# Performance work log

Hardware: AMD Instinct MI355X
Metric: run time of the kernel (lower is better)

Reference implementation:

```python
import jax, jax.numpy as jnp
import numpy as np

SEQ, B, D_IN, H = 512, 64, 256, 1024

def setup_inputs() -> dict:
    key = jax.random.key(0)
    k1, k2, k3, k4 = jax.random.split(key, 4)
    x = jax.random.normal(k1, (SEQ, B, D_IN), dtype=jnp.float32)
    W_in = jax.random.normal(k2, (H, D_IN), dtype=jnp.float32) / np.sqrt(D_IN)
    W_hh = jax.random.normal(k3, (H, H), dtype=jnp.float32) / np.sqrt(H)
    bias = jnp.zeros((H,), dtype=jnp.float32)
    alpha = jax.random.uniform(k4, (H,), dtype=jnp.float32)
    return {"x": x, "W_in": W_in, "W_hh": W_hh, "bias": bias, "alpha": alpha}

def reference(x, W_in, W_hh, bias, alpha):
    # x: [S, B, D_in]; returns (output [S, B, H], h_n [B, H])
    S, B_, _ = x.shape
    H_ = W_hh.shape[0]
    # Precompute input projection for all timesteps in one GEMM: [S, B, H]
    x_proj = jnp.einsum('sbi,hi->sbh', x, W_in) + bias

    def step(h_prev, xp_t):
        h_tilde = jnp.tanh(xp_t + h_prev @ W_hh.T)
        h = (1.0 - alpha) * h_prev + alpha * h_tilde
        return h, h

    h0 = jnp.zeros((B_, H_), dtype=x.dtype)
    h_n, output = jax.lax.scan(step, h0, x_proj)
    return output, h_n
```

## Files before the change

### kernel.cpp

```cpp
#include <hip/hip_runtime.h>
#include <hip/hip_cooperative_groups.h>
#include <cstdint>
#include <cstddef>

#define SEQ   512
#define BATCH 64
#define DIN   256
#define HDIM  1024
#define NGROUP 8
#define GROWS  8
#define NSLAB  32

typedef __attribute__((ext_vector_type(8)))  short  short8;
typedef __attribute__((ext_vector_type(4)))  float  float4v;
typedef __attribute__((ext_vector_type(2)))  float  float2v;

__device__ __forceinline__ short f2bf(float f) {
    union { float f; uint32_t u; } v; v.f = f;
    uint32_t u = v.u;
    uint32_t r = (u + 0x7fffu + ((u >> 16) & 1u)) >> 16;
    return (short)(r & 0xffffu);
}
__device__ __forceinline__ float bf2f(short s) {
    union { uint32_t u; float f; } v; v.u = ((uint32_t)(uint16_t)s) << 16;
    return v.f;
}

__global__ void prep_kernel(const float* __restrict__ W_hh,
                            short* __restrict__ w_hi,
                            short* __restrict__ w_lo,
                            short* __restrict__ hbuf,
                            unsigned int* __restrict__ prog) {
    int tid = blockIdx.x * blockDim.x + threadIdx.x;
    int stride = gridDim.x * blockDim.x;
    for (int i = tid; i < HDIM * HDIM; i += stride) {
        float w = W_hh[i];
        short hi = f2bf(w);
        float lo = w - bf2f(hi);
        w_hi[i] = hi;
        w_lo[i] = f2bf(lo);
    }
    for (int i = tid; i < 2 * BATCH * HDIM; i += stride) hbuf[i] = 0;
    for (int i = tid; i < NGROUP * NSLAB; i += stride) prog[i] = 0u;
}

#define XBM 128
#define XBN 128
#define XBK 32

__global__ __launch_bounds__(256) void xproj_kernel(
    const float* __restrict__ X,
    const float* __restrict__ Win,
    const float* __restrict__ bias,
    float* __restrict__ out)
{
    __shared__ float As[XBK][XBM + 4];
    __shared__ float Bs[XBK][XBN + 4];
    const int bm = blockIdx.x;
    const int bn = blockIdx.y;
    const int r0 = bm * XBM, c0 = bn * XBN;
    const int tid = threadIdx.x;
    const int tx = tid & 15, ty = tid >> 4;

    float acc[8][8];
#pragma unroll
    for (int i = 0; i < 8; i++)
#pragma unroll
        for (int j = 0; j < 8; j++) acc[i][j] = 0.f;

    for (int k0 = 0; k0 < DIN; k0 += XBK) {
#pragma unroll
        for (int r = 0; r < 4; r++) {
            int row = (tid >> 3) + 32 * r;
            int kk  = (tid & 7) * 4;
            float4v v = *(const float4v*)(X + (size_t)(r0 + row) * DIN + k0 + kk);
            As[kk + 0][row] = v[0]; As[kk + 1][row] = v[1];
            As[kk + 2][row] = v[2]; As[kk + 3][row] = v[3];
        }
#pragma unroll
        for (int r = 0; r < 4; r++) {
            int row = (tid >> 3) + 32 * r;
            int kk  = (tid & 7) * 4;
            float4v v = *(const float4v*)(Win + (size_t)(c0 + row) * DIN + k0 + kk);
            Bs[kk + 0][row] = v[0]; Bs[kk + 1][row] = v[1];
            Bs[kk + 2][row] = v[2]; Bs[kk + 3][row] = v[3];
        }
        __syncthreads();
#pragma unroll
        for (int k = 0; k < XBK; k++) {
            float4v a0 = *(const float4v*)&As[k][ty * 8];
            float4v a1 = *(const float4v*)&As[k][ty * 8 + 4];
            float4v b0 = *(const float4v*)&Bs[k][tx * 8];
            float4v b1 = *(const float4v*)&Bs[k][tx * 8 + 4];
            float a[8] = {a0[0],a0[1],a0[2],a0[3],a1[0],a1[1],a1[2],a1[3]};
            float b[8] = {b0[0],b0[1],b0[2],b0[3],b1[0],b1[1],b1[2],b1[3]};
#pragma unroll
            for (int i = 0; i < 8; i++)
#pragma unroll
                for (int j = 0; j < 8; j++) acc[i][j] += a[i] * b[j];
        }
        __syncthreads();
    }

    float4v ba = *(const float4v*)(bias + c0 + tx * 8);
    float4v bb = *(const float4v*)(bias + c0 + tx * 8 + 4);
#pragma unroll
    for (int i = 0; i < 8; i++) {
        size_t row = (size_t)(r0 + ty * 8 + i);
        float4v v0, v1;
#pragma unroll
        for (int j = 0; j < 4; j++) { v0[j] = acc[i][j] + ba[j]; v1[j] = acc[i][4 + j] + bb[j]; }
        *(float4v*)(out + row * HDIM + c0 + tx * 8)     = v0;
        *(float4v*)(out + row * HDIM + c0 + tx * 8 + 4) = v1;
    }
}

__global__ __launch_bounds__(512, 2) void rnn2_kernel(
    const float* __restrict__ alpha,
    const short* __restrict__ w_hi,
    const short* __restrict__ w_lo,
    short* __restrict__ hbuf,
    unsigned int* __restrict__ prog,
    float* __restrict__ out)
{
    __shared__ float zbuf[8][2][16][16];

    const int blk  = blockIdx.x;
    const int g    = blk >> 5;
    const int j    = blk & 31;
    const int tid  = threadIdx.x;
    const int wave = tid >> 6;
    const int lane = tid & 63;
    const int kq   = wave;
    const int ln15 = lane & 15;
    const int kg   = lane >> 4;
    const int k_base = kq * 128 + kg * 8;
    const bool mvalid = (ln15 < GROWS);

    short8 wf[2][4][2];
#pragma unroll
    for (int nt = 0; nt < 2; nt++)
#pragma unroll
        for (int kt = 0; kt < 4; kt++) {
            int col = j * 32 + nt * 16 + ln15;
            int k   = k_base + kt * 32;
            wf[nt][kt][0] = *(const short8*)(w_hi + (size_t)col * HDIM + k);
            wf[nt][kt][1] = *(const short8*)(w_lo + (size_t)col * HDIM + k);
        }

    const int em = tid >> 4;
    const int cp = (tid & 15) * 2;
    const int erow = g * GROWS + em;
    const int egc  = j * 32 + cp;
    float hp0 = 0.f, hp1 = 0.f;
    float2v al = {0.f, 0.f};
    if (tid < 128) al = *(const float2v*)(alpha + egc);

    const int arow = g * GROWS + ln15;

    for (int t = 0; t < SEQ; t++) {
        const int cur = t & 1, nxt = cur ^ 1;

        float4v acc0 = {0.f,0.f,0.f,0.f}, acc1 = {0.f,0.f,0.f,0.f};
#pragma unroll
        for (int kt = 0; kt < 4; kt++) {
            short8 ahi = (short8)0, alo = (short8)0;
            if (mvalid) {
                const unsigned long long* phi = (const unsigned long long*)
                    (hbuf + ((size_t)(cur*2+0)*BATCH + arow)*HDIM + k_base + kt*32);
                const unsigned long long* plo = (const unsigned long long*)
                    (hbuf + ((size_t)(cur*2+1)*BATCH + arow)*HDIM + k_base + kt*32);
                union { unsigned long long u[2]; short8 s; } uh, ul;
                uh.u[0] = __hip_atomic_load(phi,   __ATOMIC_RELAXED, __HIP_MEMORY_SCOPE_AGENT);
                uh.u[1] = __hip_atomic_load(phi+1, __ATOMIC_RELAXED, __HIP_MEMORY_SCOPE_AGENT);
                ul.u[0] = __hip_atomic_load(plo,   __ATOMIC_RELAXED, __HIP_MEMORY_SCOPE_AGENT);
                ul.u[1] = __hip_atomic_load(plo+1, __ATOMIC_RELAXED, __HIP_MEMORY_SCOPE_AGENT);
                ahi = uh.s; alo = ul.s;
            }
            acc0 = __builtin_amdgcn_mfma_f32_16x16x32_bf16(ahi, wf[0][kt][0], acc0, 0, 0, 0);
            acc0 = __builtin_amdgcn_mfma_f32_16x16x32_bf16(ahi, wf[0][kt][1], acc0, 0, 0, 0);
            acc0 = __builtin_amdgcn_mfma_f32_16x16x32_bf16(alo, wf[0][kt][0], acc0, 0, 0, 0);
            acc1 = __builtin_amdgcn_mfma_f32_16x16x32_bf16(ahi, wf[1][kt][0], acc1, 0, 0, 0);
            acc1 = __builtin_amdgcn_mfma_f32_16x16x32_bf16(ahi, wf[1][kt][1], acc1, 0, 0, 0);
            acc1 = __builtin_amdgcn_mfma_f32_16x16x32_bf16(alo, wf[1][kt][0], acc1, 0, 0, 0);
        }
#pragma unroll
        for (int reg = 0; reg < 4; reg++) {
            int m = kg * 4 + reg;
            zbuf[kq][0][m][ln15] = acc0[reg];
            zbuf[kq][1][m][ln15] = acc1[reg];
        }
        __syncthreads();

        if (tid < 128) {
            float z0 = 0.f, z1 = 0.f;
            const int nt0 = cp >> 4, n0 = cp & 15;
#pragma unroll
            for (int q = 0; q < 8; q++) {
                z0 += zbuf[q][nt0][em][n0];
                z1 += zbuf[q][nt0][em][n0 + 1];
            }
            size_t oidx = (size_t)t * (BATCH * HDIM) + (size_t)erow * HDIM + egc;
            float2v xp = *(const float2v*)(out + oidx);
            float ht0 = tanhf(z0 + xp[0]);
            float ht1 = tanhf(z1 + xp[1]);
            hp0 = (1.0f - al[0]) * hp0 + al[0] * ht0;
            hp1 = (1.0f - al[1]) * hp1 + al[1] * ht1;
            float2v res = {hp0, hp1};
            *(float2v*)(out + oidx) = res;
            if (t == SEQ - 1) {
                *(float2v*)(out + (size_t)SEQ * BATCH * HDIM + (size_t)erow * HDIM + egc) = res;
            }
            short h0 = f2bf(hp0), h1 = f2bf(hp1);
            short l0 = f2bf(hp0 - bf2f(h0)), l1 = f2bf(hp1 - bf2f(h1));
            uint32_t packh = (uint32_t)(uint16_t)h0 | ((uint32_t)(uint16_t)h1 << 16);
            uint32_t packl = (uint32_t)(uint16_t)l0 | ((uint32_t)(uint16_t)l1 << 16);
            uint32_t* dhi = (uint32_t*)(hbuf + ((size_t)(nxt*2+0)*BATCH + erow)*HDIM + egc);
            uint32_t* dlo = (uint32_t*)(hbuf + ((size_t)(nxt*2+1)*BATCH + erow)*HDIM + egc);
            __hip_atomic_store(dhi, packh, __ATOMIC_RELAXED, __HIP_MEMORY_SCOPE_AGENT);
            __hip_atomic_store(dlo, packl, __ATOMIC_RELAXED, __HIP_MEMORY_SCOPE_AGENT);
        }

        if (t < SEQ - 1) {
            __builtin_amdgcn_s_waitcnt(0);
            __syncthreads();
            if (tid == 0) {
                __hip_atomic_store(&prog[blk], (unsigned int)(t + 1),
                                   __ATOMIC_RELAXED, __HIP_MEMORY_SCOPE_AGENT);
            }
            if (tid < NSLAB) {
                while (__hip_atomic_load(&prog[g * NSLAB + tid],
                                         __ATOMIC_RELAXED, __HIP_MEMORY_SCOPE_AGENT)
                       < (unsigned int)(t + 1)) {
                    __builtin_amdgcn_s_sleep(1);
                }
            }
            __syncthreads();
        }
    }
}

extern "C" void kernel_launch(void* const* d_in, const int* in_sizes, int n_in,
                              void* d_out, int out_size, void* d_ws, size_t ws_size,
                              hipStream_t stream) {
    const float* x     = (const float*)d_in[0];
    const float* W_in  = (const float*)d_in[1];
    const float* W_hh  = (const float*)d_in[2];
    const float* bias  = (const float*)d_in[3];
    const float* alpha = (const float*)d_in[4];
    float* out = (float*)d_out;

    short* w_hi = (short*)d_ws;
    short* w_lo = w_hi + (size_t)HDIM * HDIM;
    short* hbuf = w_lo + (size_t)HDIM * HDIM;
    unsigned int* prog = (unsigned int*)(hbuf + (size_t)2 * 2 * BATCH * HDIM);

    prep_kernel<<<512, 256, 0, stream>>>(W_hh, w_hi, w_lo, hbuf, prog);

    dim3 xg(SEQ * BATCH / XBM, HDIM / XBN);
    xproj_kernel<<<xg, 256, 0, stream>>>(x, W_in, bias, out);

    void* args[] = { (void*)&alpha, (void*)&w_hi, (void*)&w_lo,
                     (void*)&hbuf, (void*)&prog, (void*)&out };
    (void)hipLaunchCooperativeKernel((const void*)rnn2_kernel,
                                     dim3(NGROUP * NSLAB), dim3(512),
                                     args, 0, stream);
}
```

Before: 2.791 ms.

## Replace progress-counter barrier with tag-in-data polling on hidden-state buffers

Drops the per-step progress counter and spin-wait barrier. Consumers now poll the hidden-state buffers directly, checking a 2-bit step tag embedded in the low mantissa bits of element 0 of each 4-element packet, so synchronisation rides on the data loads. It also swaps tanhf for an exp/rcp fast tanh, widens the epilogue to one wave writing 4 columns with 64-bit packed stores, prefetches x_proj before the wait, double-buffers zbuf, and remaps blocks so consecutive blocks share a row group. It risks slight precision loss from the tag bits and fast tanh, relies on 64-bit stores landing atomically, and uses a bounded spin guard that could read stale data.

```diff
diff --git a/kernel.cpp b/kernel.cpp
--- a/kernel.cpp
+++ b/kernel.cpp
@@ -1,5 +1,4 @@
 #include <hip/hip_runtime.h>
-#include <hip/hip_cooperative_groups.h>
 #include <cstdint>
 #include <cstddef>
 
@@ -13,7 +12,6 @@
 
 typedef __attribute__((ext_vector_type(8)))  short  short8;
 typedef __attribute__((ext_vector_type(4)))  float  float4v;
-typedef __attribute__((ext_vector_type(2)))  float  float2v;
 
 __device__ __forceinline__ short f2bf(float f) {
     union { float f; uint32_t u; } v; v.f = f;
@@ -25,12 +23,17 @@
     union { uint32_t u; float f; } v; v.u = ((uint32_t)(uint16_t)s) << 16;
     return v.f;
 }
+__device__ __forceinline__ float fast_tanh(float x) {
+    float ax = __builtin_fabsf(x);
+    float e  = __expf(-2.0f * ax);
+    float r  = (1.0f - e) * __builtin_amdgcn_rcpf(1.0f + e);
+    return __builtin_copysignf(r, x);
+}
 
 __global__ void prep_kernel(const float* __restrict__ W_hh,
                             short* __restrict__ w_hi,
                             short* __restrict__ w_lo,
-                            short* __restrict__ hbuf,
-                            unsigned int* __restrict__ prog) {
+                            short* __restrict__ hbuf) {
     int tid = blockIdx.x * blockDim.x + threadIdx.x;
     int stride = gridDim.x * blockDim.x;
     for (int i = tid; i < HDIM * HDIM; i += stride) {
@@ -40,8 +43,7 @@
         w_hi[i] = hi;
         w_lo[i] = f2bf(lo);
     }
-    for (int i = tid; i < 2 * BATCH * HDIM; i += stride) hbuf[i] = 0;
-    for (int i = tid; i < NGROUP * NSLAB; i += stride) prog[i] = 0u;
+    for (int i = tid; i < 2 * 2 * BATCH * HDIM; i += stride) hbuf[i] = 0;
 }
 
 #define XBM 128
@@ -115,27 +117,26 @@
     }
 }
 
-__global__ __launch_bounds__(512, 2) void rnn2_kernel(
+__global__ __launch_bounds__(512, 1) void rnn4_kernel(
     const float* __restrict__ alpha,
     const short* __restrict__ w_hi,
     const short* __restrict__ w_lo,
     short* __restrict__ hbuf,
-    unsigned int* __restrict__ prog,
     float* __restrict__ out)
 {
-    __shared__ float zbuf[8][2][16][16];
+    __shared__ float zbuf[2][8][2][8][20];
 
     const int blk  = blockIdx.x;
-    const int g    = blk >> 5;
-    const int j    = blk & 31;
+    const int g    = blk & 7;
+    const int j    = blk >> 3;
     const int tid  = threadIdx.x;
     const int wave = tid >> 6;
     const int lane = tid & 63;
+
     const int kq   = wave;
     const int ln15 = lane & 15;
     const int kg   = lane >> 4;
     const int k_base = kq * 128 + kg * 8;
-    const bool mvalid = (ln15 < GROWS);
 
     short8 wf[2][4][2];
 #pragma unroll
@@ -148,94 +149,112 @@
             wf[nt][kt][1] = *(const short8*)(w_lo + (size_t)col * HDIM + k);
         }
 
-    const int em = tid >> 4;
-    const int cp = (tid & 15) * 2;
+    const int ar = g * GROWS + (ln15 & 7);
+
+    const int em = lane >> 3;
+    const int c0 = (lane & 7) * 4;
     const int erow = g * GROWS + em;
-    const int egc  = j * 32 + cp;
-    float hp0 = 0.f, hp1 = 0.f;
-    float2v al = {0.f, 0.f};
-    if (tid < 128) al = *(const float2v*)(alpha + egc);
-
-    const int arow = g * GROWS + ln15;
+    const int egc  = j * 32 + c0;
+    const int nt0 = c0 >> 4, n0 = c0 & 15;
+    float hp[4] = {0.f, 0.f, 0.f, 0.f};
+    float4v al4 = {0.f, 0.f, 0.f, 0.f};
+    if (wave == 0) al4 = *(const float4v*)(alpha + egc);
 
     for (int t = 0; t < SEQ; t++) {
-        const int cur = t & 1, nxt = cur ^ 1;
+        const int cur = t & 1, nxt = cur ^ 1, par = cur;
+
+        float4v xpn = {0.f, 0.f, 0.f, 0.f};
+        float* xaddr = out + (size_t)t * (BATCH * HDIM) + (size_t)erow * HDIM + egc;
+        if (wave == 0) xpn = *(const float4v*)xaddr;
+
+        const short* bh = hbuf + ((size_t)(cur * 2 + 0) * BATCH + ar) * HDIM + k_base;
+        const short* bl = hbuf + ((size_t)(cur * 2 + 1) * BATCH + ar) * HDIM + k_base;
+        const unsigned long long etag =
+            (unsigned long long)((((unsigned)(t - 1) >> 1) % 3u) + 1u);
+        union HU { unsigned long long u[2]; short8 s; } uh[4], ul[4];
+        int ok, guard = 0;
+        do {
+            ok = 1;
+#pragma unroll
+            for (int kt = 0; kt < 4; kt++) {
+                const unsigned long long* ph = (const unsigned long long*)(bh + kt * 32);
+                const unsigned long long* pl = (const unsigned long long*)(bl + kt * 32);
+                uh[kt].u[0] = __hip_atomic_load(ph,     __ATOMIC_RELAXED, __HIP_MEMORY_SCOPE_AGENT);
+                uh[kt].u[1] = __hip_atomic_load(ph + 1, __ATOMIC_RELAXED, __HIP_MEMORY_SCOPE_AGENT);
+                ul[kt].u[0] = __hip_atomic_load(pl,     __ATOMIC_RELAXED, __HIP_MEMORY_SCOPE_AGENT);
+                ul[kt].u[1] = __hip_atomic_load(pl + 1, __ATOMIC_RELAXED, __HIP_MEMORY_SCOPE_AGENT);
+            }
+            if (t > 0) {
+#pragma unroll
+                for (int kt = 0; kt < 4; kt++) {
+                    ok &= (int)((uh[kt].u[0] & 3ull) == etag) & (int)((uh[kt].u[1] & 3ull) == etag);
+                    ok &= (int)((ul[kt].u[0] & 3ull) == etag) & (int)((ul[kt].u[1] & 3ull) == etag);
+                }
+            }
+        } while (!ok && ++guard < (1 << 14));
 
         float4v acc0 = {0.f,0.f,0.f,0.f}, acc1 = {0.f,0.f,0.f,0.f};
 #pragma unroll
         for (int kt = 0; kt < 4; kt++) {
-            short8 ahi = (short8)0, alo = (short8)0;
-            if (mvalid) {
-                const unsigned long long* phi = (const unsigned long long*)
-                    (hbuf + ((size_t)(cur*2+0)*BATCH + arow)*HDIM + k_base + kt*32);
-                const unsigned long long* plo = (const unsigned long long*)
-                    (hbuf + ((size_t)(cur*2+1)*BATCH + arow)*HDIM + k_base + kt*32);
-                union { unsigned long long u[2]; short8 s; } uh, ul;
-                uh.u[0] = __hip_atomic_load(phi,   __ATOMIC_RELAXED, __HIP_MEMORY_SCOPE_AGENT);
-                uh.u[1] = __hip_atomic_load(phi+1, __ATOMIC_RELAXED, __HIP_MEMORY_SCOPE_AGENT);
-                ul.u[0] = __hip_atomic_load(plo,   __ATOMIC_RELAXED, __HIP_MEMORY_SCOPE_AGENT);
-                ul.u[1] = __hip_atomic_load(plo+1, __ATOMIC_RELAXED, __HIP_MEMORY_SCOPE_AGENT);
-                ahi = uh.s; alo = ul.s;
-            }
-            acc0 = __builtin_amdgcn_mfma_f32_16x16x32_bf16(ahi, wf[0][kt][0], acc0, 0, 0, 0);
-            acc0 = __builtin_amdgcn_mfma_f32_16x16x32_bf16(ahi, wf[0][kt][1], acc0, 0, 0, 0);
-            acc0 = __builtin_amdgcn_mfma_f32_16x16x32_bf16(alo, wf[0][kt][0], acc0, 0, 0, 0);
-            acc1 = __builtin_amdgcn_mfma_f32_16x16x32_bf16(ahi, wf[1][kt][0], acc1, 0, 0, 0);
-            acc1 = __builtin_amdgcn_mfma_f32_16x16x32_bf16(ahi, wf[1][kt][1], acc1, 0, 0, 0);
-            acc1 = __builtin_amdgcn_mfma_f32_16x16x32_bf16(alo, wf[1][kt][0], acc1, 0, 0, 0);
-        }
-#pragma unroll
-        for (int reg = 0; reg < 4; reg++) {
-            int m = kg * 4 + reg;
-            zbuf[kq][0][m][ln15] = acc0[reg];
-            zbuf[kq][1][m][ln15] = acc1[reg];
+            acc0 = __builtin_amdgcn_mfma_f32_16x16x32_bf16(uh[kt].s, wf[0][kt][0], acc0, 0, 0, 0);
+            acc0 = __builtin_amdgcn_mfma_f32_16x16x32_bf16(uh[kt].s, wf[0][kt][1], acc0, 0, 0, 0);
+            acc0 = __builtin_amdgcn_mfma_f32_16x16x32_bf16(ul[kt].s, wf[0][kt][0], acc0, 0, 0, 0);
+            acc1 = __builtin_amdgcn_mfma_f32_16x16x32_bf16(uh[kt].s, wf[1][kt][0], acc1, 0, 0, 0);
+            acc1 = __builtin_amdgcn_mfma_f32_16x16x32_bf16(uh[kt].s, wf[1][kt][1], acc1, 0, 0, 0);
+            acc1 = __builtin_amdgcn_mfma_f32_16x16x32_bf16(ul[kt].s, wf[1][kt][0], acc1, 0, 0, 0);
+        }
+        if (kg < 2) {
+#pragma unroll
+            for (int reg = 0; reg < 4; reg++) {
+                int m = kg * 4 + reg;
+                zbuf[par][kq][0][m][ln15] = acc0[reg];
+                zbuf[par][kq][1][m][ln15] = acc1[reg];
+            }
         }
         __syncthreads();
 
-        if (tid < 128) {
-            float z0 = 0.f, z1 = 0.f;
-            const int nt0 = cp >> 4, n0 = cp & 15;
+        if (wave == 0) {
+            float4v z = {0.f, 0.f, 0.f, 0.f};
 #pragma unroll
             for (int q = 0; q < 8; q++) {
-                z0 += zbuf[q][nt0][em][n0];
-                z1 += zbuf[q][nt0][em][n0 + 1];
-            }
-            size_t oidx = (size_t)t * (BATCH * HDIM) + (size_t)erow * HDIM + egc;
-            float2v xp = *(const float2v*)(out + oidx);
-            float ht0 = tanhf(z0 + xp[0]);
-            float ht1 = tanhf(z1 + xp[1]);
-            hp0 = (1.0f - al[0]) * hp0 + al[0] * ht0;
-            hp1 = (1.0f - al[1]) * hp1 + al[1] * ht1;
-            float2v res = {hp0, hp1};
-            *(float2v*)(out + oidx) = res;
-            if (t == SEQ - 1) {
-                *(float2v*)(out + (size_t)SEQ * BATCH * HDIM + (size_t)erow * HDIM + egc) = res;
-            }
-            short h0 = f2bf(hp0), h1 = f2bf(hp1);
-            short l0 = f2bf(hp0 - bf2f(h0)), l1 = f2bf(hp1 - bf2f(h1));
-            uint32_t packh = (uint32_t)(uint16_t)h0 | ((uint32_t)(uint16_t)h1 << 16);
-            uint32_t packl = (uint32_t)(uint16_t)l0 | ((uint32_t)(uint16_t)l1 << 16);
-            uint32_t* dhi = (uint32_t*)(hbuf + ((size_t)(nxt*2+0)*BATCH + erow)*HDIM + egc);
-            uint32_t* dlo = (uint32_t*)(hbuf + ((size_t)(nxt*2+1)*BATCH + erow)*HDIM + egc);
+                float4v zz = *(const float4v*)&zbuf[par][q][nt0][em][n0];
+                z += zz;
+            }
+#pragma unroll
+            for (int i = 0; i < 4; i++) {
+                float ht = fast_tanh(z[i] + xpn[i]);
+                hp[i] = hp[i] + al4[i] * (ht - hp[i]);
+            }
+            const unsigned wtag = (((unsigned)t >> 1) % 3u) + 1u;
+            short h0 = f2bf(hp[0]);
+            h0 = (short)(((unsigned short)h0 & ~3u) | wtag);
+            short h1 = f2bf(hp[1]), h2 = f2bf(hp[2]), h3 = f2bf(hp[3]);
+            short l0 = f2bf(hp[0] - bf2f(h0));
+            short l1 = f2bf(hp[1] - bf2f(h1));
+            short l2 = f2bf(hp[2] - bf2f(h2));
+            short l3 = f2bf(hp[3] - bf2f(h3));
+            l0 = (short)(((unsigned short)l0 & ~3u) | wtag);
+            unsigned long long packh =
+                  (unsigned long long)(unsigned short)h0
+                | ((unsigned long long)(unsigned short)h1 << 16)
+                | ((unsigned long long)(unsigned short)h2 << 32)
+                | ((unsigned long long)(unsigned short)h3 << 48);
+            unsigned long long packl =
+                  (unsigned long long)(unsigned short)l0
+                | ((unsigned long long)(unsigned short)l1 << 16)
+                | ((unsigned long long)(unsigned short)l2 << 32)
+                | ((unsigned long long)(unsigned short)l3 << 48);
+            unsigned long long* dhi =
+                (unsigned long long*)(hbuf + ((size_t)(nxt * 2 + 0) * BATCH + erow) * HDIM + egc);
+            unsigned long long* dlo =
+                (unsigned long long*)(hbuf + ((size_t)(nxt * 2 + 1) * BATCH + erow) * HDIM + egc);
             __hip_atomic_store(dhi, packh, __ATOMIC_RELAXED, __HIP_MEMORY_SCOPE_AGENT);
             __hip_atomic_store(dlo, packl, __ATOMIC_RELAXED, __HIP_MEMORY_SCOPE_AGENT);
-        }
-
-        if (t < SEQ - 1) {
-            __builtin_amdgcn_s_waitcnt(0);
-            __syncthreads();
-            if (tid == 0) {
-                __hip_atomic_store(&prog[blk], (unsigned int)(t + 1),
-                                   __ATOMIC_RELAXED, __HIP_MEMORY_SCOPE_AGENT);
-            }
-            if (tid < NSLAB) {
-                while (__hip_atomic_load(&prog[g * NSLAB + tid],
-                                         __ATOMIC_RELAXED, __HIP_MEMORY_SCOPE_AGENT)
-                       < (unsigned int)(t + 1)) {
-                    __builtin_amdgcn_s_sleep(1);
-                }
-            }
-            __syncthreads();
+
+            float4v resv = {hp[0], hp[1], hp[2], hp[3]};
+            *(float4v*)xaddr = resv;
+            if (t == SEQ - 1)
+                *(float4v*)(out + (size_t)SEQ * BATCH * HDIM + (size_t)erow * HDIM + egc) = resv;
         }
     }
 }
@@ -253,16 +272,15 @@
     short* w_hi = (short*)d_ws;
     short* w_lo = w_hi + (size_t)HDIM * HDIM;
     short* hbuf = w_lo + (size_t)HDIM * HDIM;
-    unsigned int* prog = (unsigned int*)(hbuf + (size_t)2 * 2 * BATCH * HDIM);
-
-    prep_kernel<<<512, 256, 0, stream>>>(W_hh, w_hi, w_lo, hbuf, prog);
+
+    prep_kernel<<<512, 256, 0, stream>>>(W_hh, w_hi, w_lo, hbuf);
 
     dim3 xg(SEQ * BATCH / XBM, HDIM / XBN);
     xproj_kernel<<<xg, 256, 0, stream>>>(x, W_in, bias, out);
 
     void* args[] = { (void*)&alpha, (void*)&w_hi, (void*)&w_lo,
-                     (void*)&hbuf, (void*)&prog, (void*)&out };
-    (void)hipLaunchCooperativeKernel((const void*)rnn2_kernel,
+                     (void*)&hbuf, (void*)&out };
+    (void)hipLaunchCooperativeKernel((const void*)rnn4_kernel,
                                      dim3(NGROUP * NSLAB), dim3(512),
                                      args, 0, stream);
 }
```

Result: slower. 4.658 ms (+66.9%).
